# Performance work log

Measured on AMD Instinct MI355X. Metric: run time of the kernel, lower is better.

## Reference

```python
import jax, jax.numpy as jnp
import numpy as np

EMBED = 512
HEADS = 8
HEAD_DIM = EMBED // HEADS


def setup_inputs() -> dict:
    key = jax.random.key(0)
    ks = jax.random.split(key, 9)
    B, P, S, E = 32, 512, 1024, EMBED
    query = jax.random.normal(ks[0], (B, P, E), dtype=jnp.float32)
    k_in = jax.random.normal(ks[1], (B, S, E), dtype=jnp.float32)
    v_in = jax.random.normal(ks[2], (B, S, E), dtype=jnp.float32)
    key_padding_mask = jax.random.randint(ks[3], (B, P, S), 0, 2).astype(bool)
    sc = 1.0 / np.sqrt(E)
    Wq = jax.random.normal(ks[4], (E, E), dtype=jnp.float32) * sc
    Wk = jax.random.normal(ks[5], (E, E), dtype=jnp.float32) * sc
    Wv = jax.random.normal(ks[6], (E, E), dtype=jnp.float32) * sc
    Wo = jax.random.normal(ks[7], (E, E), dtype=jnp.float32) * sc
    bo = jax.random.normal(ks[8], (E,), dtype=jnp.float32) * 0.01
    return {"query": query, "key": k_in, "value": v_in,
            "key_padding_mask": key_padding_mask,
            "Wq": Wq, "Wk": Wk, "Wv": Wv, "Wo": Wo, "bo": bo}


def reference(query, key, value, key_padding_mask, Wq, Wk, Wv, Wo, bo):
    B, P, E = query.shape
    S = key.shape[1]
    H, D = HEADS, HEAD_DIM
    scale = D ** -0.5
    # Linear projections (torch Linear: x @ W.T)
    Q = (query @ Wq.T).reshape(B, P, H, D).transpose(0, 2, 1, 3)  # [B,H,P,D]
    K = (key @ Wk.T).reshape(B, S, H, D).transpose(0, 2, 1, 3)    # [B,H,S,D]
    V = (value @ Wv.T).reshape(B, S, H, D).transpose(0, 2, 1, 3)  # [B,H,S,D]
    scores = jnp.einsum('bhpd,bhsd->bhps', Q, K) * scale          # [B,H,P,S]
    mask = key_padding_mask[:, None, :, :]                        # [B,1,P,S]
    scores = jnp.where(mask, -jnp.inf, scores)
    attn = jax.nn.softmax(scores, axis=-1)
    ctx = jnp.einsum('bhps,bhsd->bhpd', attn, V)                  # [B,H,P,D]
    ctx = ctx.transpose(0, 2, 1, 3).reshape(B, P, E)
    return ctx @ Wo.T + bo
```

## Files before the change

### kernel.cpp

```cpp
#include <hip/hip_runtime.h>

#define B_  32
#define P_  512
#define S_  1024
#define E_  512
#define H_  8
#define D_  64

typedef unsigned int uint32;
typedef unsigned short u16;
typedef __attribute__((ext_vector_type(8))) _Float16 half8;
typedef __attribute__((ext_vector_type(2))) __fp16 fp16x2;
typedef __attribute__((ext_vector_type(4))) float f32x4;
typedef __attribute__((ext_vector_type(2))) uint32 u32x2;

__device__ __forceinline__ u16 f2h_bits(float f){
  _Float16 h = (_Float16)f;
  union { _Float16 h; u16 u; } cv; cv.h = h; return cv.u;
}
__device__ __forceinline__ uint32 pk16(float a, float b){
  union { fp16x2 h; uint32 u; } cv;
  cv.h = __builtin_amdgcn_cvt_pkrtz(a, b);
  return cv.u;
}
__device__ __forceinline__ half8 cvt8(f32x4 a, f32x4 b){
  half8 h;
  h[0]=(_Float16)a[0]; h[1]=(_Float16)a[1]; h[2]=(_Float16)a[2]; h[3]=(_Float16)a[3];
  h[4]=(_Float16)b[0]; h[5]=(_Float16)b[1]; h[6]=(_Float16)b[2]; h[7]=(_Float16)b[3];
  return h;
}
__device__ __forceinline__ f32x4 mfma16(half8 a, half8 b, f32x4 c){
  return __builtin_amdgcn_mfma_f32_16x16x32_f16(a, b, c, 0, 0, 0);
}
#define GLD16(ldsp, gp) __builtin_amdgcn_global_load_lds( \
    (const __attribute__((address_space(1))) void*)(gp), \
    (__attribute__((address_space(3))) void*)(ldsp), 16, 0, 0)

__global__ void cvt_kv_kernel(const float* __restrict__ key, const float* __restrict__ value,
                              u16* __restrict__ Kh, u16* __restrict__ Vh){
  size_t i = (size_t)blockIdx.x * 256 + threadIdx.x;
  int region = (int)(i >> 21);
  size_t off = (i & 2097151) * 8;
  const float* s = region ? value : key;
  u16* d = region ? Vh : Kh;
  f32x4 a = *(const f32x4*)(s + off);
  f32x4 b = *(const f32x4*)(s + off + 4);
  *(half8*)(d + off) = cvt8(a, b);
}

__global__ void cvt_w_kernel(const float* __restrict__ w0, const float* __restrict__ w1,
                             const float* __restrict__ w2, const float* __restrict__ w3,
                             u16* __restrict__ out){
  int i = blockIdx.x * 256 + threadIdx.x;
  int region = i >> 15;
  int off = (i & 32767) * 8;
  const float* s = (region == 0) ? w0 : (region == 1) ? w1 : (region == 2) ? w2 : w3;
  f32x4 a = *(const f32x4*)(s + off);
  f32x4 b = *(const f32x4*)(s + off + 4);
  *(half8*)(out + region * 262144 + off) = cvt8(a, b);
}

__global__ void detect_mask_kernel(const uint32* __restrict__ m, int* __restrict__ flag){
  __shared__ int s_gt1, s_bgt1;
  if (threadIdx.x == 0){ s_gt1 = 0; s_bgt1 = 0; }
  __syncthreads();
  int gt1 = 0, bgt1 = 0;
  for (int i = threadIdx.x; i < 4096; i += 256){
    uint32 w = m[i];
    if (w > 1u) gt1 = 1;
    if (((w)&0xffu) > 1u || ((w>>8)&0xffu) > 1u || ((w>>16)&0xffu) > 1u || ((w>>24)&0xffu) > 1u) bgt1 = 1;
  }
  if (gt1)  atomicOr(&s_gt1, 1);
  if (bgt1) atomicOr(&s_bgt1, 1);
  __syncthreads();
  if (threadIdx.x == 0) *flag = s_gt1 ? (s_bgt1 ? 2 : 1) : 0;
}

__global__ void pack_mask_kernel(const uint32* __restrict__ m, const int* __restrict__ flag,
                                 uint32* __restrict__ bits){
  const int w = blockIdx.x * 256 + threadIdx.x;
  const int f = *flag;
  uint32 out = 0u;
  if (f == 1){
    #pragma unroll
    for (int i = 0; i < 8; i++){
      uint32 v = m[(size_t)w*8 + i];
      if (v & 0x000000ffu) out |= 1u << (i*4 + 0);
      if (v & 0x0000ff00u) out |= 1u << (i*4 + 1);
      if (v & 0x00ff0000u) out |= 1u << (i*4 + 2);
      if (v & 0xff000000u) out |= 1u << (i*4 + 3);
    }
  } else {
    #pragma unroll
    for (int i = 0; i < 32; i++){
      if (m[(size_t)w*32 + i]) out |= 1u << i;
    }
  }
  bits[w] = out;
}

template<int MODE, int A16, int B16, int SWZ>
__global__ __launch_bounds__(256) void gemm_f(
    const void* __restrict__ Ap, const void* __restrict__ Bp,
    void* __restrict__ Cp, const float* __restrict__ bias, int rshift)
{
  __shared__ __align__(16) u16 As[128*64];
  __shared__ __align__(16) u16 Bs[128*64];
  const int tid  = threadIdx.x;
  const int lane = tid & 63;
  const int wv   = tid >> 6;
  const int lrow = lane & 15, khi = lane >> 4;
  const int wm   = wv >> 1,  wn  = wv & 1;

  int bx = blockIdx.x, by = blockIdx.y;
  if (SWZ){
    const int nbx = gridDim.x;
    const int nwg = nbx * gridDim.y;
    const int bid = by * nbx + bx;
    const int l = (bid & 7) * (nwg >> 3) + (bid >> 3);
    by = l / nbx; bx = l - by * nbx;
  }
  const long gm0 = (long)by * 128;
  const long gn0 = (long)bx * 128;

  f32x4 acc[4][4];
  #pragma unroll
  for (int i = 0; i < 4; i++)
    #pragma unroll
    for (int j = 0; j < 4; j++) acc[i][j] = (f32x4){0.f,0.f,0.f,0.f};

  #pragma unroll 1
  for (int kk = 0; kk < 512; kk += 64){
    if (kk) __syncthreads();
    if (A16){
      const u16* ab = (const u16*)Ap;
      #pragma unroll
      for (int j = 0; j < 4; j++){
        int row = j*32 + (tid >> 3);
        GLD16(&As[j*2048 + tid*8], ab + (gm0 + row)*512 + kk + (tid & 7)*8);
      }
    } else {
      const float* ap = (const float*)Ap + (gm0 + (tid>>1))*512 + kk + (tid&1)*32;
      const int lidx = (tid>>1)*64 + (tid&1)*32;
      #pragma unroll
      for (int i = 0; i < 4; i++){
        f32x4 f0 = *(const f32x4*)(ap + i*8);
        f32x4 f1 = *(const f32x4*)(ap + i*8 + 4);
        *(half8*)&As[lidx + i*8] = cvt8(f0, f1);
      }
    }
    if (B16){
      const u16* bb = (const u16*)Bp;
      #pragma unroll
      for (int j = 0; j < 4; j++){
        int row = j*32 + (tid >> 3);
        GLD16(&Bs[j*2048 + tid*8], bb + (gn0 + row)*512 + kk + (tid & 7)*8);
      }
    } else {
      const float* bp = (const float*)Bp + (gn0 + (tid>>1))*512 + kk + (tid&1)*32;
      const int lidx = (tid>>1)*64 + (tid&1)*32;
      #pragma unroll
      for (int i = 0; i < 4; i++){
        f32x4 f0 = *(const f32x4*)(bp + i*8);
        f32x4 f1 = *(const f32x4*)(bp + i*8 + 4);
        *(half8*)&Bs[lidx + i*8] = cvt8(f0, f1);
      }
    }
    __syncthreads();

    half8 af[4][2], bf[4][2];
    #pragma unroll
    for (int mi = 0; mi < 4; mi++){
      const u16* p = &As[(wm*64 + mi*16 + lrow)*64 + khi*8];
      af[mi][0] = *(const half8*)p;
      af[mi][1] = *(const half8*)(p + 32);
    }
    #pragma unroll
    for (int ni = 0; ni < 4; ni++){
      const u16* p = &Bs[(wn*64 + ni*16 + lrow)*64 + khi*8];
      bf[ni][0] = *(const half8*)p;
      bf[ni][1] = *(const half8*)(p + 32);
    }
    #pragma unroll
    for (int mi = 0; mi < 4; mi++)
      #pragma unroll
      for (int ni = 0; ni < 4; ni++){
        acc[mi][ni] = mfma16(af[mi][0], bf[ni][0], acc[mi][ni]);
        acc[mi][ni] = mfma16(af[mi][1], bf[ni][1], acc[mi][ni]);
      }
  }

  #pragma unroll
  for (int mi = 0; mi < 4; mi++)
    #pragma unroll
    for (int ni = 0; ni < 4; ni++)
      #pragma unroll
      for (int r = 0; r < 4; r++){
        long gm = gm0 + wm*64 + mi*16 + khi*4 + r;
        long gn = gn0 + wn*64 + ni*16 + lrow;
        float v = acc[mi][ni][r];
        if (MODE == 0){
          long b  = gm >> rshift;
          long rr = gm & ((1L << rshift) - 1);
          long h  = gn >> 6, d = gn & 63;
          ((u16*)Cp)[((b*8 + h) << (rshift + 6)) + rr*64 + d] = f2h_bits(v);
        } else if (MODE == 1){
          long b = gn >> 10, s = gn & 1023;
          ((u16*)Cp)[b*524288 + gm*1024 + s] = f2h_bits(v);
        } else {
          ((float*)Cp)[gm*512 + gn] = v + bias[gn];
        }
      }
}

__device__ __forceinline__ int swz(int row, int col){ return row*64 + (col ^ ((row & 7) << 3)); }

__global__ __launch_bounds__(256) void attn_kernel(
    const u16* __restrict__ Qb, const u16* __restrict__ Kb,
    const u16* __restrict__ Vtb, const uint32* __restrict__ bits,
    u16* __restrict__ Ctx)
{
  __shared__ __align__(16) u16 Ks[64*64];
  __shared__ __align__(16) u16 Vs[64*64];
  __shared__ uint32 mlds[64][2];

  const int tid  = threadIdx.x;
  const int lane = tid & 63;
  const int wv   = tid >> 6;
  const int lrow = lane & 15, khi = lane >> 4;

  const int bidx = blockIdx.x;
  const int logical = (bidx & 7) * 256 + (bidx >> 3);
  const int bh = logical >> 3;
  const int p0 = (logical & 7) * 64;
  const int bb = bh >> 3;

  const u16* qp = Qb  + (size_t)bh * (P_*64) + (size_t)p0 * 64;
  const u16* kp = Kb  + (size_t)bh * (S_*64);
  const u16* vp = Vtb + (size_t)bh * (D_*S_);

  {
    int row = tid >> 2, cb = (tid & 3) * 16;
    const u16* src = qp + (size_t)row*64 + cb;
    *(half8*)&Ks[swz(row, cb)]     = *(const half8*)src;
    *(half8*)&Ks[swz(row, cb + 8)] = *(const half8*)(src + 8);
  }
  __syncthreads();
  half8 q_lo, q_hi;
  {
    const int row = wv*16 + lrow;
    q_lo = *(const half8*)&Ks[swz(row, khi*8)];
    q_hi = *(const half8*)&Ks[swz(row, khi*8 + 32)];
  }

  f32x4 accO[4];
  #pragma unroll
  for (int i = 0; i < 4; i++) accO[i] = (f32x4){0.f,0.f,0.f,0.f};
  float mst = -1e30f, lst = 0.f;

  const float SCL = 0.125f * 1.44269504f;
  const int srcA = (lrow + 16*((2*khi)    & 3)) << 2;
  const int srcB = (lrow + 16*((2*khi + 1)& 3)) << 2;
  const bool hiH = khi >= 2;

  #pragma unroll 1
  for (int s0 = 0; s0 < S_; s0 += 64){
    __syncthreads();
    {
      int row = tid >> 2, cb = (tid & 3) * 16;
      const u16* ksrc = kp + (size_t)(s0 + row)*64 + cb;
      *(half8*)&Ks[swz(row, cb)]     = *(const half8*)ksrc;
      *(half8*)&Ks[swz(row, cb + 8)] = *(const half8*)(ksrc + 8);
      const u16* vsrc = vp + (size_t)row*S_ + s0 + cb;
      *(half8*)&Vs[swz(row, cb)]     = *(const half8*)vsrc;
      *(half8*)&Vs[swz(row, cb + 8)] = *(const half8*)(vsrc + 8);
    }
    if (tid < 128){
      int row = tid >> 1, wsel = tid & 1;
      mlds[row][wsel] = bits[(size_t)(bb*P_ + p0 + row)*(S_/32) + (s0 >> 5) + wsel];
    }
    __syncthreads();

    f32x4 sc[4];
    #pragma unroll
    for (int ssub = 0; ssub < 4; ssub++){
      const int rr = ssub*16 + lrow;
      half8 k_lo = *(const half8*)&Ks[swz(rr, khi*8)];
      half8 k_hi = *(const half8*)&Ks[swz(rr, khi*8 + 32)];
      f32x4 c = (f32x4){0.f,0.f,0.f,0.f};
      c = mfma16(k_lo, q_lo, c);
      c = mfma16(k_hi, q_hi, c);
      sc[ssub] = c;
    }

    const uint32 mw0 = mlds[wv*16 + lrow][0];
    const uint32 mw1 = mlds[wv*16 + lrow][1];
    float mx = -1e30f;
    #pragma unroll
    for (int ssub = 0; ssub < 4; ssub++){
      const uint32 mw = (ssub < 2) ? mw0 : mw1;
      #pragma unroll
      for (int r = 0; r < 4; r++){
        const int s = ssub*16 + khi*4 + r;
        float v = sc[ssub][r] * SCL;
        if ((mw >> (s & 31)) & 1u) v = -1e30f;
        sc[ssub][r] = v;
        mx = fmaxf(mx, v);
      }
    }
    mx = fmaxf(mx, __shfl_xor(mx, 16));
    mx = fmaxf(mx, __shfl_xor(mx, 32));
    const float mnew = fmaxf(mst, mx);
    const float fac = __builtin_amdgcn_exp2f(mst - mnew);
    float ts = 0.f;
    #pragma unroll
    for (int ssub = 0; ssub < 4; ssub++)
      #pragma unroll
      for (int r = 0; r < 4; r++){
        float p = __builtin_amdgcn_exp2f(sc[ssub][r] - mnew);
        sc[ssub][r] = p;
        ts += p;
      }
    ts += __shfl_xor(ts, 16);
    ts += __shfl_xor(ts, 32);
    lst = lst * fac + ts;
    mst = mnew;
    #pragma unroll
    for (int d = 0; d < 4; d++){
      f32x4 a = accO[d];
      a[0] *= fac; a[1] *= fac; a[2] *= fac; a[3] *= fac;
      accO[d] = a;
    }

    uint32 w00 = pk16(sc[0][0], sc[0][1]), w01 = pk16(sc[0][2], sc[0][3]);
    uint32 w10 = pk16(sc[1][0], sc[1][1]), w11 = pk16(sc[1][2], sc[1][3]);
    uint32 w20 = pk16(sc[2][0], sc[2][1]), w21 = pk16(sc[2][2], sc[2][3]);
    uint32 w30 = pk16(sc[3][0], sc[3][1]), w31 = pk16(sc[3][2], sc[3][3]);

    union { half8 h; uint32 u[4]; } plo, phi;
    {
      uint32 t0 = __builtin_amdgcn_ds_bpermute(srcA, (int)w00);
      uint32 t1 = __builtin_amdgcn_ds_bpermute(srcA, (int)w10);
      plo.u[0] = hiH ? t1 : t0;
      t0 = __builtin_amdgcn_ds_bpermute(srcA, (int)w01);
      t1 = __builtin_amdgcn_ds_bpermute(srcA, (int)w11);
      plo.u[1] = hiH ? t1 : t0;
      t0 = __builtin_amdgcn_ds_bpermute(srcB, (int)w00);
      t1 = __builtin_amdgcn_ds_bpermute(srcB, (int)w10);
      plo.u[2] = hiH ? t1 : t0;
      t0 = __builtin_amdgcn_ds_bpermute(srcB, (int)w01);
      t1 = __builtin_amdgcn_ds_bpermute(srcB, (int)w11);
      plo.u[3] = hiH ? t1 : t0;
      t0 = __builtin_amdgcn_ds_bpermute(srcA, (int)w20);
      t1 = __builtin_amdgcn_ds_bpermute(srcA, (int)w30);
      phi.u[0] = hiH ? t1 : t0;
      t0 = __builtin_amdgcn_ds_bpermute(srcA, (int)w21);
      t1 = __builtin_amdgcn_ds_bpermute(srcA, (int)w31);
      phi.u[1] = hiH ? t1 : t0;
      t0 = __builtin_amdgcn_ds_bpermute(srcB, (int)w20);
      t1 = __builtin_amdgcn_ds_bpermute(srcB, (int)w30);
      phi.u[2] = hiH ? t1 : t0;
      t0 = __builtin_amdgcn_ds_bpermute(srcB, (int)w21);
      t1 = __builtin_amdgcn_ds_bpermute(srcB, (int)w31);
      phi.u[3] = hiH ? t1 : t0;
    }

    #pragma unroll
    for (int dsub = 0; dsub < 4; dsub++){
      const int rr = dsub*16 + lrow;
      half8 v_lo = *(const half8*)&Vs[swz(rr, khi*8)];
      half8 v_hi = *(const half8*)&Vs[swz(rr, khi*8 + 32)];
      accO[dsub] = mfma16(v_lo, plo.h, accO[dsub]);
      accO[dsub] = mfma16(v_hi, phi.h, accO[dsub]);
    }
  }

  const int hh = bh & 7;
  const float inv = __builtin_amdgcn_rcpf(lst);
  const size_t base = (size_t)(bb*P_ + p0 + wv*16 + lrow) * E_ + hh*64 + khi*4;
  #pragma unroll
  for (int dsub = 0; dsub < 4; dsub++){
    u32x2 pkd;
    pkd.x = pk16(accO[dsub][0] * inv, accO[dsub][1] * inv);
    pkd.y = pk16(accO[dsub][2] * inv, accO[dsub][3] * inv);
    *(u32x2*)&Ctx[base + dsub*16] = pkd;
  }
}

extern "C" void kernel_launch(void* const* d_in, const int* in_sizes, int n_in,
                              void* d_out, int out_size, void* d_ws, size_t ws_size,
                              hipStream_t stream)
{
  const float* query = (const float*)d_in[0];
  const float* key   = (const float*)d_in[1];
  const float* value = (const float*)d_in[2];
  const void*  mask  = d_in[3];
  const float* Wq = (const float*)d_in[4];
  const float* Wk = (const float*)d_in[5];
  const float* Wv = (const float*)d_in[6];
  const float* Wo = (const float*)d_in[7];
  const float* bo = (const float*)d_in[8];

  char* ws = (char*)d_ws;
  u16*    Vh   = (u16*)(ws);
  u16*    Kh   = (u16*)(ws + (32u << 20));
  u16*    Kb   = (u16*)(ws + (64u << 20));
  u16*    Vtb  = (u16*)(ws + (32u << 20));
  u16*    Qb   = (u16*)(ws);
  u16*    Ctx  = (u16*)(ws + (16u << 20));
  u16*    W4h  = (u16*)(ws + (96u << 20));
  uint32* bits = (uint32*)d_out;
  int*    flag = (int*)((char*)d_out + (2u << 20));

  cvt_kv_kernel<<<16384, 256, 0, stream>>>(key, value, Kh, Vh);
  cvt_w_kernel<<<512, 256, 0, stream>>>(Wq, Wk, Wv, Wo, W4h);
  detect_mask_kernel<<<1, 256, 0, stream>>>((const uint32*)mask, flag);
  pack_mask_kernel<<<2048, 256, 0, stream>>>((const uint32*)mask, flag, bits);
  gemm_f<0,1,1,1><<<dim3(4, 256), 256, 0, stream>>>((const void*)Kh, (const void*)(W4h + 262144),
                                                    (void*)Kb, nullptr, 10);
  gemm_f<1,1,1,0><<<dim3(256, 4), 256, 0, stream>>>((const void*)(W4h + 524288), (const void*)Vh,
                                                    (void*)Vtb, nullptr, 0);
  gemm_f<0,0,1,1><<<dim3(4, 128), 256, 0, stream>>>((const void*)query, (const void*)W4h,
                                                    (void*)Qb, nullptr, 9);
  attn_kernel<<<2048, 256, 0, stream>>>(Qb, Kb, Vtb, bits, Ctx);
  gemm_f<2,1,1,1><<<dim3(4, 128), 256, 0, stream>>>((const void*)Ctx, (const void*)(W4h + 786432),
                                                    d_out, bo, 0);
}
```

Baseline: 430.9 us.

## Fuse fp32 conversion into projection GEMMs, prefetch K/V in registers, lazy softmax rescale

Drops the separate K/V fp32-to-fp16 conversion pass and has the projection GEMMs convert activations while staging them, with a pre-swizzled weight layout to avoid LDS bank conflicts. Folds the softmax scale into the Q projection and vectorizes the Q/K output stores. In attention, the next K/V tile and mask words are prefetched into registers, MFMA sections get raised wave priority, and the running-max rescale happens only when the max grows by more than a threshold. This cuts a full read/write of K and V plus per-tile rescale work, at the cost of extra register pressure and a looser softmax stabilization bound.

```diff
diff --git a/kernel.cpp b/kernel.cpp
--- a/kernel.cpp
+++ b/kernel.cpp
@@ -32,21 +32,10 @@
 __device__ __forceinline__ f32x4 mfma16(half8 a, half8 b, f32x4 c){
   return __builtin_amdgcn_mfma_f32_16x16x32_f16(a, b, c, 0, 0, 0);
 }
+__device__ __forceinline__ int swz(int row, int col){ return row*64 + (col ^ ((row & 7) << 3)); }
 #define GLD16(ldsp, gp) __builtin_amdgcn_global_load_lds( \
     (const __attribute__((address_space(1))) void*)(gp), \
     (__attribute__((address_space(3))) void*)(ldsp), 16, 0, 0)
-
-__global__ void cvt_kv_kernel(const float* __restrict__ key, const float* __restrict__ value,
-                              u16* __restrict__ Kh, u16* __restrict__ Vh){
-  size_t i = (size_t)blockIdx.x * 256 + threadIdx.x;
-  int region = (int)(i >> 21);
-  size_t off = (i & 2097151) * 8;
-  const float* s = region ? value : key;
-  u16* d = region ? Vh : Kh;
-  f32x4 a = *(const f32x4*)(s + off);
-  f32x4 b = *(const f32x4*)(s + off + 4);
-  *(half8*)(d + off) = cvt8(a, b);
-}
 
 __global__ void cvt_w_kernel(const float* __restrict__ w0, const float* __restrict__ w1,
                              const float* __restrict__ w2, const float* __restrict__ w3,
@@ -57,7 +46,10 @@
   const float* s = (region == 0) ? w0 : (region == 1) ? w1 : (region == 2) ? w2 : w3;
   f32x4 a = *(const f32x4*)(s + off);
   f32x4 b = *(const f32x4*)(s + off + 4);
-  *(half8*)(out + region * 262144 + off) = cvt8(a, b);
+  int row = off >> 9;
+  int k   = off & 511;
+  int ks  = (region < 3) ? ((k & ~63) | ((k & 63) ^ ((row & 7) << 3))) : k;
+  *(half8*)(out + region * 262144 + row*512 + ks) = cvt8(a, b);
 }
 
 __global__ void detect_mask_kernel(const uint32* __restrict__ m, int* __restrict__ flag){
@@ -99,10 +91,10 @@
   bits[w] = out;
 }
 
-template<int MODE, int A16, int B16, int SWZ>
-__global__ __launch_bounds__(256) void gemm_f(
-    const void* __restrict__ Ap, const void* __restrict__ Bp,
-    void* __restrict__ Cp, const float* __restrict__ bias, int rshift)
+template<int MODE>
+__global__ __launch_bounds__(256) void gemm_proj(
+    const u16* __restrict__ Wsz, const float* __restrict__ Act,
+    u16* __restrict__ Cp, int rshift, float scale)
 {
   __shared__ __align__(16) u16 As[128*64];
   __shared__ __align__(16) u16 Bs[128*64];
@@ -112,8 +104,102 @@
   const int lrow = lane & 15, khi = lane >> 4;
   const int wm   = wv >> 1,  wn  = wv & 1;
 
+  const int nwg = gridDim.x;
+  const int bid = blockIdx.x;
+  const int l   = (bid & 7) * (nwg >> 3) + (bid >> 3);
+  const int by  = l & 3;
+  const long bxL = l >> 2;
+
+  const long gm0 = (long)by * 128;
+  const long gn0 = bxL * 128;
+  const int  srow = tid >> 1, scb = (tid & 1) * 32;
+
+  f32x4 acc[4][4];
+  #pragma unroll
+  for (int i = 0; i < 4; i++)
+    #pragma unroll
+    for (int j = 0; j < 4; j++) acc[i][j] = (f32x4){0.f,0.f,0.f,0.f};
+
+  #pragma unroll 1
+  for (int kk = 0; kk < 512; kk += 64){
+    if (kk) __syncthreads();
+    #pragma unroll
+    for (int j = 0; j < 4; j++){
+      int row = j*32 + (tid >> 3);
+      GLD16(&As[j*2048 + tid*8], Wsz + (gm0 + row)*512 + kk + (tid & 7)*8);
+    }
+    {
+      const float* bp = Act + (gn0 + srow)*512 + kk + scb;
+      #pragma unroll
+      for (int i = 0; i < 4; i++){
+        f32x4 f0 = *(const f32x4*)(bp + i*8);
+        f32x4 f1 = *(const f32x4*)(bp + i*8 + 4);
+        *(half8*)&Bs[swz(srow, scb + i*8)] = cvt8(f0, f1);
+      }
+    }
+    __syncthreads();
+
+    half8 af[4][2], bf[4][2];
+    #pragma unroll
+    for (int mi = 0; mi < 4; mi++){
+      const int r_ = wm*64 + mi*16 + lrow;
+      af[mi][0] = *(const half8*)&As[swz(r_, khi*8)];
+      af[mi][1] = *(const half8*)&As[swz(r_, khi*8 + 32)];
+    }
+    #pragma unroll
+    for (int ni = 0; ni < 4; ni++){
+      const int r_ = wn*64 + ni*16 + lrow;
+      bf[ni][0] = *(const half8*)&Bs[swz(r_, khi*8)];
+      bf[ni][1] = *(const half8*)&Bs[swz(r_, khi*8 + 32)];
+    }
+    #pragma unroll
+    for (int mi = 0; mi < 4; mi++)
+      #pragma unroll
+      for (int ni = 0; ni < 4; ni++){
+        acc[mi][ni] = mfma16(af[mi][0], bf[ni][0], acc[mi][ni]);
+        acc[mi][ni] = mfma16(af[mi][1], bf[ni][1], acc[mi][ni]);
+      }
+  }
+
+  #pragma unroll
+  for (int mi = 0; mi < 4; mi++)
+    #pragma unroll
+    for (int ni = 0; ni < 4; ni++){
+      f32x4 v = acc[mi][ni];
+      const long arow = gn0 + wn*64 + ni*16 + lrow;
+      if (MODE == 0){
+        const int h  = (int)(gm0 >> 6) + wm;
+        const int d0 = mi*16 + khi*4;
+        const long b  = arow >> rshift;
+        const long rr = arow & ((1L << rshift) - 1);
+        u32x2 p;
+        p.x = pk16(v[0]*scale, v[1]*scale);
+        p.y = pk16(v[2]*scale, v[3]*scale);
+        *(u32x2*)&Cp[(((b*8 + h) << rshift) + rr)*64 + d0] = p;
+      } else {
+        const long n = gm0 + wm*64 + mi*16 + khi*4;
+        const long b = arow >> 10, s = arow & 1023;
+        #pragma unroll
+        for (int r = 0; r < 4; r++)
+          Cp[b*524288 + (n + r)*1024 + s] = f2h_bits(v[r]);
+      }
+    }
+}
+
+__global__ __launch_bounds__(256) void gemm_out(
+    const u16* __restrict__ Ap, const u16* __restrict__ Bp,
+    float* __restrict__ Cp, const float* __restrict__ bias)
+{
+  __shared__ __align__(16) u16 As[128*64];
+  __shared__ __align__(16) u16 Bs[128*64];
+  const int tid  = threadIdx.x;
+  const int lane = tid & 63;
+  const int wv   = tid >> 6;
+  const int lrow = lane & 15, khi = lane >> 4;
+  const int wm   = wv >> 1,  wn  = wv & 1;
+
   int bx = blockIdx.x, by = blockIdx.y;
-  if (SWZ){
+  {
     const int nbx = gridDim.x;
     const int nwg = nbx * gridDim.y;
     const int bid = by * nbx + bx;
@@ -132,39 +218,11 @@
   #pragma unroll 1
   for (int kk = 0; kk < 512; kk += 64){
     if (kk) __syncthreads();
-    if (A16){
-      const u16* ab = (const u16*)Ap;
-      #pragma unroll
-      for (int j = 0; j < 4; j++){
-        int row = j*32 + (tid >> 3);
-        GLD16(&As[j*2048 + tid*8], ab + (gm0 + row)*512 + kk + (tid & 7)*8);
-      }
-    } else {
-      const float* ap = (const float*)Ap + (gm0 + (tid>>1))*512 + kk + (tid&1)*32;
-      const int lidx = (tid>>1)*64 + (tid&1)*32;
-      #pragma unroll
-      for (int i = 0; i < 4; i++){
-        f32x4 f0 = *(const f32x4*)(ap + i*8);
-        f32x4 f1 = *(const f32x4*)(ap + i*8 + 4);
-        *(half8*)&As[lidx + i*8] = cvt8(f0, f1);
-      }
-    }
-    if (B16){
-      const u16* bb = (const u16*)Bp;
-      #pragma unroll
-      for (int j = 0; j < 4; j++){
-        int row = j*32 + (tid >> 3);
-        GLD16(&Bs[j*2048 + tid*8], bb + (gn0 + row)*512 + kk + (tid & 7)*8);
-      }
-    } else {
-      const float* bp = (const float*)Bp + (gn0 + (tid>>1))*512 + kk + (tid&1)*32;
-      const int lidx = (tid>>1)*64 + (tid&1)*32;
-      #pragma unroll
-      for (int i = 0; i < 4; i++){
-        f32x4 f0 = *(const f32x4*)(bp + i*8);
-        f32x4 f1 = *(const f32x4*)(bp + i*8 + 4);
-        *(half8*)&Bs[lidx + i*8] = cvt8(f0, f1);
-      }
+    #pragma unroll
+    for (int j = 0; j < 4; j++){
+      int row = j*32 + (tid >> 3);
+      GLD16(&As[j*2048 + tid*8], Ap + (gm0 + row)*512 + kk + (tid & 7)*8);
+      GLD16(&Bs[j*2048 + tid*8], Bp + (gn0 + row)*512 + kk + (tid & 7)*8);
     }
     __syncthreads();
 
@@ -198,22 +256,9 @@
       for (int r = 0; r < 4; r++){
         long gm = gm0 + wm*64 + mi*16 + khi*4 + r;
         long gn = gn0 + wn*64 + ni*16 + lrow;
-        float v = acc[mi][ni][r];
-        if (MODE == 0){
-          long b  = gm >> rshift;
-          long rr = gm & ((1L << rshift) - 1);
-          long h  = gn >> 6, d = gn & 63;
-          ((u16*)Cp)[((b*8 + h) << (rshift + 6)) + rr*64 + d] = f2h_bits(v);
-        } else if (MODE == 1){
-          long b = gn >> 10, s = gn & 1023;
-          ((u16*)Cp)[b*524288 + gm*1024 + s] = f2h_bits(v);
-        } else {
-          ((float*)Cp)[gm*512 + gn] = v + bias[gn];
-        }
-      }
-}
-
-__device__ __forceinline__ int swz(int row, int col){ return row*64 + (col ^ ((row & 7) << 3)); }
+        Cp[gm*512 + gn] = acc[mi][ni][r] + bias[gn];
+      }
+}
 
 __global__ __launch_bounds__(256) void attn_kernel(
     const u16* __restrict__ Qb, const u16* __restrict__ Kb,
@@ -222,7 +267,6 @@
 {
   __shared__ __align__(16) u16 Ks[64*64];
   __shared__ __align__(16) u16 Vs[64*64];
-  __shared__ uint32 mlds[64][2];
 
   const int tid  = threadIdx.x;
   const int lane = tid & 63;
@@ -238,50 +282,52 @@
   const u16* qp = Qb  + (size_t)bh * (P_*64) + (size_t)p0 * 64;
   const u16* kp = Kb  + (size_t)bh * (S_*64);
   const u16* vp = Vtb + (size_t)bh * (D_*S_);
+  const int srow = tid >> 2, scb = (tid & 3) * 16;
+  const size_t mbase = (size_t)(bb*P_ + p0 + wv*16 + lrow) * (S_/32);
+
+  half8 kr0 = *(const half8*)(kp + (size_t)srow*64 + scb);
+  half8 kr1 = *(const half8*)(kp + (size_t)srow*64 + scb + 8);
+  half8 vr0 = *(const half8*)(vp + (size_t)srow*S_ + scb);
+  half8 vr1 = *(const half8*)(vp + (size_t)srow*S_ + scb + 8);
+  uint32 mw0 = bits[mbase], mw1 = bits[mbase + 1];
 
   {
-    int row = tid >> 2, cb = (tid & 3) * 16;
-    const u16* src = qp + (size_t)row*64 + cb;
-    *(half8*)&Ks[swz(row, cb)]     = *(const half8*)src;
-    *(half8*)&Ks[swz(row, cb + 8)] = *(const half8*)(src + 8);
+    const u16* src = qp + (size_t)srow*64 + scb;
+    *(half8*)&Ks[swz(srow, scb)]     = *(const half8*)src;
+    *(half8*)&Ks[swz(srow, scb + 8)] = *(const half8*)(src + 8);
   }
   __syncthreads();
-  half8 q_lo, q_hi;
-  {
-    const int row = wv*16 + lrow;
-    q_lo = *(const half8*)&Ks[swz(row, khi*8)];
-    q_hi = *(const half8*)&Ks[swz(row, khi*8 + 32)];
-  }
+  half8 q_lo = *(const half8*)&Ks[swz(wv*16 + lrow, khi*8)];
+  half8 q_hi = *(const half8*)&Ks[swz(wv*16 + lrow, khi*8 + 32)];
 
   f32x4 accO[4];
   #pragma unroll
   for (int i = 0; i < 4; i++) accO[i] = (f32x4){0.f,0.f,0.f,0.f};
   float mst = -1e30f, lst = 0.f;
 
-  const float SCL = 0.125f * 1.44269504f;
   const int srcA = (lrow + 16*((2*khi)    & 3)) << 2;
   const int srcB = (lrow + 16*((2*khi + 1)& 3)) << 2;
   const bool hiH = khi >= 2;
 
   #pragma unroll 1
-  for (int s0 = 0; s0 < S_; s0 += 64){
+  for (int t = 0; t < 16; t++){
     __syncthreads();
-    {
-      int row = tid >> 2, cb = (tid & 3) * 16;
-      const u16* ksrc = kp + (size_t)(s0 + row)*64 + cb;
-      *(half8*)&Ks[swz(row, cb)]     = *(const half8*)ksrc;
-      *(half8*)&Ks[swz(row, cb + 8)] = *(const half8*)(ksrc + 8);
-      const u16* vsrc = vp + (size_t)row*S_ + s0 + cb;
-      *(half8*)&Vs[swz(row, cb)]     = *(const half8*)vsrc;
-      *(half8*)&Vs[swz(row, cb + 8)] = *(const half8*)(vsrc + 8);
-    }
-    if (tid < 128){
-      int row = tid >> 1, wsel = tid & 1;
-      mlds[row][wsel] = bits[(size_t)(bb*P_ + p0 + row)*(S_/32) + (s0 >> 5) + wsel];
-    }
+    *(half8*)&Ks[swz(srow, scb)]     = kr0;
+    *(half8*)&Ks[swz(srow, scb + 8)] = kr1;
+    *(half8*)&Vs[swz(srow, scb)]     = vr0;
+    *(half8*)&Vs[swz(srow, scb + 8)] = vr1;
     __syncthreads();
+    const uint32 cm0 = mw0, cm1 = mw1;
+    if (t < 15){
+      const u16* kn = kp + (size_t)(t + 1)*4096 + (size_t)srow*64 + scb;
+      kr0 = *(const half8*)kn; kr1 = *(const half8*)(kn + 8);
+      const u16* vn = vp + (size_t)srow*S_ + (t + 1)*64 + scb;
+      vr0 = *(const half8*)vn; vr1 = *(const half8*)(vn + 8);
+      mw0 = bits[mbase + (t + 1)*2]; mw1 = bits[mbase + (t + 1)*2 + 1];
+    }
 
     f32x4 sc[4];
+    __builtin_amdgcn_s_setprio(1);
     #pragma unroll
     for (int ssub = 0; ssub < 4; ssub++){
       const int rr = ssub*16 + lrow;
@@ -292,17 +338,16 @@
       c = mfma16(k_hi, q_hi, c);
       sc[ssub] = c;
     }
-
-    const uint32 mw0 = mlds[wv*16 + lrow][0];
-    const uint32 mw1 = mlds[wv*16 + lrow][1];
+    __builtin_amdgcn_s_setprio(0);
+
     float mx = -1e30f;
     #pragma unroll
     for (int ssub = 0; ssub < 4; ssub++){
-      const uint32 mw = (ssub < 2) ? mw0 : mw1;
+      const uint32 mw = (ssub < 2) ? cm0 : cm1;
       #pragma unroll
       for (int r = 0; r < 4; r++){
         const int s = ssub*16 + khi*4 + r;
-        float v = sc[ssub][r] * SCL;
+        float v = sc[ssub][r];
         if ((mw >> (s & 31)) & 1u) v = -1e30f;
         sc[ssub][r] = v;
         mx = fmaxf(mx, v);
@@ -310,27 +355,30 @@
     }
     mx = fmaxf(mx, __shfl_xor(mx, 16));
     mx = fmaxf(mx, __shfl_xor(mx, 32));
-    const float mnew = fmaxf(mst, mx);
-    const float fac = __builtin_amdgcn_exp2f(mst - mnew);
+    if (__any(mx - mst > 8.f)){
+      const float mnew = fmaxf(mst, mx);
+      const float fac = __builtin_amdgcn_exp2f(mst - mnew);
+      lst *= fac;
+      #pragma unroll
+      for (int d = 0; d < 4; d++){
+        f32x4 a = accO[d];
+        a[0] *= fac; a[1] *= fac; a[2] *= fac; a[3] *= fac;
+        accO[d] = a;
+      }
+      mst = mnew;
+    }
     float ts = 0.f;
     #pragma unroll
     for (int ssub = 0; ssub < 4; ssub++)
       #pragma unroll
       for (int r = 0; r < 4; r++){
-        float p = __builtin_amdgcn_exp2f(sc[ssub][r] - mnew);
+        float p = __builtin_amdgcn_exp2f(sc[ssub][r] - mst);
         sc[ssub][r] = p;
         ts += p;
       }
     ts += __shfl_xor(ts, 16);
     ts += __shfl_xor(ts, 32);
-    lst = lst * fac + ts;
-    mst = mnew;
-    #pragma unroll
-    for (int d = 0; d < 4; d++){
-      f32x4 a = accO[d];
-      a[0] *= fac; a[1] *= fac; a[2] *= fac; a[3] *= fac;
-      accO[d] = a;
-    }
+    lst += ts;
 
     uint32 w00 = pk16(sc[0][0], sc[0][1]), w01 = pk16(sc[0][2], sc[0][3]);
     uint32 w10 = pk16(sc[1][0], sc[1][1]), w11 = pk16(sc[1][2], sc[1][3]);
@@ -339,8 +387,9 @@
 
     union { half8 h; uint32 u[4]; } plo, phi;
     {
-      uint32 t0 = __builtin_amdgcn_ds_bpermute(srcA, (int)w00);
-      uint32 t1 = __builtin_amdgcn_ds_bpermute(srcA, (int)w10);
+      uint32 t0, t1;
+      t0 = __builtin_amdgcn_ds_bpermute(srcA, (int)w00);
+      t1 = __builtin_amdgcn_ds_bpermute(srcA, (int)w10);
       plo.u[0] = hiH ? t1 : t0;
       t0 = __builtin_amdgcn_ds_bpermute(srcA, (int)w01);
       t1 = __builtin_amdgcn_ds_bpermute(srcA, (int)w11);
@@ -365,6 +414,7 @@
       phi.u[3] = hiH ? t1 : t0;
     }
 
+    __builtin_amdgcn_s_setprio(1);
     #pragma unroll
     for (int dsub = 0; dsub < 4; dsub++){
       const int rr = dsub*16 + lrow;
@@ -373,6 +423,7 @@
       accO[dsub] = mfma16(v_lo, plo.h, accO[dsub]);
       accO[dsub] = mfma16(v_hi, phi.h, accO[dsub]);
     }
+    __builtin_amdgcn_s_setprio(0);
   }
 
   const int hh = bh & 7;
@@ -402,27 +453,22 @@
   const float* bo = (const float*)d_in[8];
 
   char* ws = (char*)d_ws;
-  u16*    Vh   = (u16*)(ws);
-  u16*    Kh   = (u16*)(ws + (32u << 20));
-  u16*    Kb   = (u16*)(ws + (64u << 20));
-  u16*    Vtb  = (u16*)(ws + (32u << 20));
   u16*    Qb   = (u16*)(ws);
-  u16*    Ctx  = (u16*)(ws + (16u << 20));
+  u16*    Kb   = (u16*)(ws + (16u << 20));
+  u16*    Vtb  = (u16*)(ws + (48u << 20));
+  u16*    Ctx  = (u16*)(ws + (80u << 20));
   u16*    W4h  = (u16*)(ws + (96u << 20));
   uint32* bits = (uint32*)d_out;
   int*    flag = (int*)((char*)d_out + (2u << 20));
 
-  cvt_kv_kernel<<<16384, 256, 0, stream>>>(key, value, Kh, Vh);
+  const float SCLQ = 0.125f * 1.44269504f;
+
   cvt_w_kernel<<<512, 256, 0, stream>>>(Wq, Wk, Wv, Wo, W4h);
   detect_mask_kernel<<<1, 256, 0, stream>>>((const uint32*)mask, flag);
   pack_mask_kernel<<<2048, 256, 0, stream>>>((const uint32*)mask, flag, bits);
-  gemm_f<0,1,1,1><<<dim3(4, 256), 256, 0, stream>>>((const void*)Kh, (const void*)(W4h + 262144),
-                                                    (void*)Kb, nullptr, 10);
-  gemm_f<1,1,1,0><<<dim3(256, 4), 256, 0, stream>>>((const void*)(W4h + 524288), (const void*)Vh,
-                                                    (void*)Vtb, nullptr, 0);
-  gemm_f<0,0,1,1><<<dim3(4, 128), 256, 0, stream>>>((const void*)query, (const void*)W4h,
-                                                    (void*)Qb, nullptr, 9);
+  gemm_proj<0><<<512, 256, 0, stream>>>(W4h, query, Qb, 9, SCLQ);
+  gemm_proj<0><<<1024, 256, 0, stream>>>(W4h + 262144, key, Kb, 10, 1.0f);
+  gemm_proj<1><<<1024, 256, 0, stream>>>(W4h + 524288, value, Vtb, 0, 1.0f);
   attn_kernel<<<2048, 256, 0, stream>>>(Qb, Kb, Vtb, bits, Ctx);
-  gemm_f<2,1,1,1><<<dim3(4, 128), 256, 0, stream>>>((const void*)Ctx, (const void*)(W4h + 786432),
-                                                    d_out, bo, 0);
-}
+  gemm_out<<<dim3(4, 128), 256, 0, stream>>>(Ctx, W4h + 786432, (float*)d_out, bo);
+}
```

After: 426.3 us. No clear change (-1.1%).
